# Kernel tuning notes

Hardware: AMD Instinct MI355X
Metric: run time of the kernel (lower is better)

Reference implementation:

```python
import jax, jax.numpy as jnp
import numpy as np

WS = (2, 8, 8)      # window size (wt, wh, ww)
SS = (1, 4, 4)      # shift size
HEADS = 6


def _window_partition(x, ws):
    B, T, H, W, C = x.shape
    wt, wh, ww = ws
    x = x.reshape(B, T // wt, wt, H // wh, wh, W // ww, ww, C)
    x = x.transpose(0, 1, 3, 5, 2, 4, 6, 7)
    return x.reshape(-1, wt * wh * ww, C)  # (B*nW, N, C)


def _window_reverse(w, ws, B, T, H, W):
    wt, wh, ww = ws
    C = w.shape[-1]
    x = w.reshape(B, T // wt, H // wh, W // ww, wt, wh, ww, C)
    x = x.transpose(0, 1, 4, 2, 5, 3, 6, 7)
    return x.reshape(B, T, H, W, C)


def _rel_pos_index(ws):
    wt, wh, ww = ws
    coords = np.stack(np.meshgrid(np.arange(wt), np.arange(wh), np.arange(ww), indexing='ij'))
    coords = coords.reshape(3, -1)                      # (3, N)
    rel = coords[:, :, None] - coords[:, None, :]       # (3, N, N)
    rel = rel.transpose(1, 2, 0).astype(np.int32)
    rel[..., 0] += wt - 1
    rel[..., 1] += wh - 1
    rel[..., 2] += ww - 1
    rel[..., 0] *= (2 * wh - 1) * (2 * ww - 1)
    rel[..., 1] *= (2 * ww - 1)
    return rel.sum(-1)                                  # (N, N)


def _shift_mask(T, H, W, ws, ss):
    # standard Swin shifted-window attention mask
    img = np.zeros((1, T, H, W, 1), dtype=np.float32)
    cnt = 0
    for t in (slice(0, -ws[0]), slice(-ws[0], -ss[0]), slice(-ss[0], None)):
        for h in (slice(0, -ws[1]), slice(-ws[1], -ss[1]), slice(-ss[1], None)):
            for w in (slice(0, -ws[2]), slice(-ws[2], -ss[2]), slice(-ss[2], None)):
                img[:, t, h, w, :] = cnt
                cnt += 1
    mw = np.asarray(_window_partition(jnp.asarray(img), ws)).squeeze(-1)  # (nW, N)
    diff = mw[:, None, :] - mw[:, :, None]
    return jnp.asarray(np.where(diff != 0, -100.0, 0.0).astype(np.float32))


def setup_inputs() -> dict:
    key = jax.random.key(0)
    ks = jax.random.split(key, 9)
    B, T, H, W, C = 2, 8, 64, 64, 192
    hid = 4 * C
    s = 0.02
    x = jax.random.normal(ks[0], (B, T, H, W, C), jnp.float32)
    qkv_w = jax.random.normal(ks[1], (3 * C, C), jnp.float32) * s
    qkv_b = jnp.zeros((3 * C,), jnp.float32)
    proj_w = jax.random.normal(ks[2], (C, C), jnp.float32) * s
    proj_b = jnp.zeros((C,), jnp.float32)
    n_rel = (2 * WS[0] - 1) * (2 * WS[1] - 1) * (2 * WS[2] - 1)
    rpb_table = jax.random.normal(ks[3], (n_rel, HEADS), jnp.float32) * s
    rpb_index = jnp.asarray(_rel_pos_index(WS))
    fc1_w = jax.random.normal(ks[4], (hid, C), jnp.float32) * s
    fc1_b = jnp.zeros((hid,), jnp.float32)
    fc2_w = jax.random.normal(ks[5], (C, hid), jnp.float32) * s
    fc2_b = jnp.zeros((C,), jnp.float32)
    attn_mask = _shift_mask(T, H, W, WS, SS)
    return dict(x=x, attn_mask=attn_mask, qkv_w=qkv_w, qkv_b=qkv_b, proj_w=proj_w,
                proj_b=proj_b, rpb_table=rpb_table, rpb_index=rpb_index,
                fc1_w=fc1_w, fc1_b=fc1_b, fc2_w=fc2_w, fc2_b=fc2_b)


def reference(x, attn_mask, qkv_w, qkv_b, proj_w, proj_b, rpb_table, rpb_index,
              fc1_w, fc1_b, fc2_w, fc2_b):
    B, T, H, W, C = x.shape
    h = HEADS
    d = C // h
    scale = d ** -0.5

    shifted = jnp.roll(x, (-SS[0], -SS[1], -SS[2]), axis=(1, 2, 3))
    xw = _window_partition(shifted, WS)            # (Bn, N, C)
    Bn, N, _ = xw.shape

    qkv = (xw @ qkv_w.T + qkv_b).reshape(Bn, N, 3, h, d).transpose(2, 0, 3, 1, 4)
    q, k, v = qkv[0], qkv[1], qkv[2]               # (Bn, h, N, d)
    attn = jnp.einsum('bhnd,bhmd->bhnm', q * scale, k)
    bias = rpb_table[rpb_index.reshape(-1)].reshape(N, N, h).transpose(2, 0, 1)
    attn = attn + bias[None]
    nW = attn_mask.shape[0]
    attn = (attn.reshape(Bn // nW, nW, h, N, N) + attn_mask[None, :, None]).reshape(Bn, h, N, N)
    attn = jax.nn.softmax(attn, axis=-1)
    out = jnp.einsum('bhnm,bhmd->bhnd', attn, v).transpose(0, 2, 1, 3).reshape(Bn, N, C)
    out = out @ proj_w.T + proj_b

    z = _window_reverse(out, WS, B, T, H, W)
    z = jnp.roll(z, (SS[0], SS[1], SS[2]), axis=(1, 2, 3))

    y = z + x
    mlp = jax.nn.gelu(y @ fc1_w.T + fc1_b, approximate=False) @ fc2_w.T + fc2_b
    return x + mlp
```

## Files before the change

kernel.cpp:

```cpp
#include <hip/hip_runtime.h>
#include <hip/hip_bf16.h>

typedef __attribute__((ext_vector_type(4))) float f32x4;
typedef __attribute__((ext_vector_type(8))) short bf16x8;

#define DEV __device__ __forceinline__

DEV unsigned short f2bf(float f) {
  union { float f; unsigned int u; } v; v.f = f;
  unsigned int r = v.u + 0x7fffu + ((v.u >> 16) & 1u);
  return (unsigned short)(r >> 16);
}

DEV float bf2f(unsigned short u) {
  union { unsigned int u; float f; } v; v.u = ((unsigned int)u) << 16; return v.f;
}

DEV short2 pkbf(float a, float b) {
  float2 t; t.x = a; t.y = b;
  __hip_bfloat162 h = __float22bfloat162_rn(t);
  union { __hip_bfloat162 h; short2 s; } u; u.h = h; return u.s;
}

DEV bf16x8 cvt8(float4 u, float4 v) {
  short2 a = pkbf(u.x, u.y), b = pkbf(u.z, u.w), c = pkbf(v.x, v.y), d = pkbf(v.z, v.w);
  bf16x8 r;
  r[0] = a.x; r[1] = a.y; r[2] = b.x; r[3] = b.y;
  r[4] = c.x; r[5] = c.y; r[6] = d.x; r[7] = d.y;
  return r;
}

DEV float gelu_fast(float v) {
  float u = 1.5957691216057308f * v * (1.0f + 0.044715f * v * v);
  return v / (1.0f + __expf(-u));
}

DEV size_t winmap(int row) {
  int wIdx = row >> 7, n = row & 127;
  int b = wIdx >> 8, widx = wIdx & 255;
  int t = (((widx >> 6) * 2 + (n >> 6)) + 1) & 7;
  int h = ((((widx >> 3) & 7) * 8 + ((n >> 3) & 7)) + 4) & 63;
  int w = (((widx & 7) * 8 + (n & 7)) + 4) & 63;
  return (size_t)(((b * 8 + t) * 64 + h) * 64 + w);
}

DEV int reg3(int tw, int hw, int ww, int n) {
  int ts = tw * 2 + (n >> 6);
  int hs = hw * 8 + ((n >> 3) & 7);
  int wsv = ww * 8 + (n & 7);
  int rt = (ts >= 7) ? 2 : ((ts >= 6) ? 1 : 0);
  int rh = (hs >= 60) ? 2 : ((hs >= 56) ? 1 : 0);
  int rw = (wsv >= 60) ? 2 : ((wsv >= 56) ? 1 : 0);
  return rt * 9 + rh * 3 + rw;
}

DEV void gload16(const unsigned short* g, unsigned short* lds) {
  __builtin_amdgcn_global_load_lds(
      (const __attribute__((address_space(1))) unsigned int*)g,
      (__attribute__((address_space(3))) unsigned int*)lds, 16, 0, 0);
}

__global__ __launch_bounds__(256) void k_prep(
    const float* __restrict__ qkv_w, const float* __restrict__ proj_w,
    const float* __restrict__ fc1_w, const float* __restrict__ fc2_w,
    const float* __restrict__ rpb_t, const int* __restrict__ rpb_i,
    unsigned short* __restrict__ wq, unsigned short* __restrict__ wp,
    unsigned short* __restrict__ w1, unsigned short* __restrict__ w2,
    float* __restrict__ b6) {
  int i = blockIdx.x * 256 + threadIdx.x;
  if (i < 110592) wq[i] = f2bf(qkv_w[i]);
  if (i < 36864)  wp[i] = f2bf(proj_w[i]);
  if (i < 147456) { w1[i] = f2bf(fc1_w[i]); w2[i] = f2bf(fc2_w[i]); }
  if (i < 16384) {
    int idx = rpb_i[i];
    #pragma unroll
    for (int h = 0; h < 6; ++h) b6[h * 16384 + i] = rpb_t[idx * 6 + h];
  }
}

__global__ __launch_bounds__(256) void k_qkv(
    const float* __restrict__ x, const unsigned short* __restrict__ Bm,
    const float* __restrict__ bias, unsigned short* __restrict__ outb) {
  __shared__ char smem[40960];
  float* As = (float*)smem;
  unsigned short* Bs = (unsigned short*)(smem + 32768);
  unsigned short* Cs = (unsigned short*)smem;
  const int tid = threadIdx.x;
  const int wave = tid >> 6, lane = tid & 63;
  const int lin = ((int)blockIdx.x & 7) * 576 + ((int)blockIdx.x >> 3);
  const int mt = lin / 9, nt = lin - mt * 9;
  const int m0 = mt * 128, n0 = nt * 64;
  const int wr = wave >> 1, wc = wave & 1;
  const int l8 = lane >> 3, s8 = lane & 7;

  const float* aptr[8];
  #pragma unroll
  for (int i = 0; i < 8; ++i) {
    int row = wave * 32 + i * 4 + (lane >> 4);
    aptr[i] = x + winmap(m0 + row) * 192 + (((lane & 15) ^ (row & 15)) << 2);
  }

  f32x4 acc[4][2] = {};
  for (int kt = 0; kt < 192; kt += 64) {
    __syncthreads();
    #pragma unroll
    for (int i = 0; i < 8; ++i)
      gload16((const unsigned short*)(aptr[i] + kt), (unsigned short*)(As + (wave * 8 + i) * 256));
    #pragma unroll
    for (int j = 0; j < 2; ++j) {
      int c = wave * 2 + j;
      int row = c * 8 + l8;
      gload16(Bm + (size_t)(n0 + row) * 192 + kt + (s8 ^ l8) * 8, Bs + c * 512);
    }
    __syncthreads();

    #pragma unroll
    for (int kk = 0; kk < 2; ++kk) {
      bf16x8 af[4], bfr[2];
      #pragma unroll
      for (int mi = 0; mi < 4; ++mi) {
        int r = wr * 64 + mi * 16 + (lane & 15);
        int s0 = kk * 8 + (lane >> 4) * 2;
        float4 u = *(const float4*)(As + r * 64 + ((s0 ^ (r & 15)) << 2));
        float4 v = *(const float4*)(As + r * 64 + (((s0 + 1) ^ (r & 15)) << 2));
        af[mi] = cvt8(u, v);
      }
      #pragma unroll
      for (int ni = 0; ni < 2; ++ni) {
        int row = wc * 32 + ni * 16 + (lane & 15);
        int slot = (kk * 4 + (lane >> 4)) ^ (row & 7);
        bfr[ni] = *(const bf16x8*)(Bs + row * 64 + slot * 8);
      }
      #pragma unroll
      for (int mi = 0; mi < 4; ++mi)
        #pragma unroll
        for (int ni = 0; ni < 2; ++ni)
          acc[mi][ni] = __builtin_amdgcn_mfma_f32_16x16x32_bf16(af[mi], bfr[ni], acc[mi][ni], 0, 0, 0);
    }
  }

  __syncthreads();
  #pragma unroll
  for (int ni = 0; ni < 2; ++ni) {
    int coll = wc * 32 + ni * 16 + (lane & 15);
    float bb = bias[n0 + coll];
    #pragma unroll
    for (int mi = 0; mi < 4; ++mi) {
      int rbase = wr * 64 + mi * 16 + ((lane >> 4) << 2);
      #pragma unroll
      for (int j = 0; j < 4; ++j)
        Cs[(rbase + j) * 72 + coll] = f2bf(acc[mi][ni][j] + bb);
    }
  }
  __syncthreads();
  const int row = tid >> 1, hh = tid & 1;
  unsigned short* gb = outb + (size_t)(m0 + row) * 576 + n0 + hh * 32;
  #pragma unroll
  for (int s = 0; s < 4; ++s)
    *(bf16x8*)(gb + s * 8) = *(const bf16x8*)(Cs + row * 72 + hh * 32 + s * 8);
}

enum { EPI_BF16 = 0, EPI_PROJ = 2 };

template <int EPI, int GATHER>
__global__ __launch_bounds__(256) void gemm_bt(
    const void* __restrict__ Ap, const unsigned short* __restrict__ Bm,
    const float* __restrict__ bias, unsigned short* __restrict__ outb,
    const float* __restrict__ xres, int N, int K, int NT) {
  __shared__ unsigned short sh[128 * 72];
  unsigned short* Bs = sh;
  const int tid = threadIdx.x;
  const int wave = tid >> 6, lane = tid & 63;
  const int total = (int)gridDim.x;
  const int lin = ((int)blockIdx.x & 7) * (total >> 3) + ((int)blockIdx.x >> 3);
  const int mt = lin / NT, nt = lin - mt * NT;
  const int m0 = mt * 128, n0 = nt * 64;
  const int wr = wave >> 1, wc = wave & 1;
  const int l8 = lane >> 3, s8 = lane & 7;
  const unsigned short* Ab = (const unsigned short*)Ap;

  size_t abase[4];
  #pragma unroll
  for (int mi = 0; mi < 4; ++mi) {
    int arow = m0 + wr * 64 + mi * 16 + (lane & 15);
    abase[mi] = (size_t)arow * K;
  }

  f32x4 acc[4][2] = {};
  for (int kt = 0; kt < K; kt += 64) {
    __syncthreads();
    #pragma unroll
    for (int i = 0; i < 2; ++i) {
      int c = wave * 2 + i;
      int row = c * 8 + l8;
      gload16(Bm + (size_t)(n0 + row) * K + kt + (s8 ^ l8) * 8, Bs + c * 512);
    }
    __syncthreads();

    #pragma unroll
    for (int kk = 0; kk < 2; ++kk) {
      bf16x8 af[4], bfr[2];
      #pragma unroll
      for (int mi = 0; mi < 4; ++mi)
        af[mi] = *(const bf16x8*)(Ab + abase[mi] + kt + kk * 32 + (lane >> 4) * 8);
      #pragma unroll
      for (int ni = 0; ni < 2; ++ni) {
        int row = wc * 32 + ni * 16 + (lane & 15);
        int slot = (kk * 4 + (lane >> 4)) ^ (row & 7);
        bfr[ni] = *(const bf16x8*)(Bs + row * 64 + slot * 8);
      }
      #pragma unroll
      for (int mi = 0; mi < 4; ++mi)
        #pragma unroll
        for (int ni = 0; ni < 2; ++ni)
          acc[mi][ni] = __builtin_amdgcn_mfma_f32_16x16x32_bf16(af[mi], bfr[ni], acc[mi][ni], 0, 0, 0);
    }
  }

  __syncthreads();
  #pragma unroll
  for (int ni = 0; ni < 2; ++ni) {
    int coll = wc * 32 + ni * 16 + (lane & 15);
    float bb = bias[n0 + coll];
    #pragma unroll
    for (int mi = 0; mi < 4; ++mi) {
      int rbase = wr * 64 + mi * 16 + ((lane >> 4) << 2);
      #pragma unroll
      for (int j = 0; j < 4; ++j)
        sh[(rbase + j) * 72 + coll] = f2bf(acc[mi][ni][j] + bb);
    }
  }
  __syncthreads();
  const int row = tid >> 1, hh = tid & 1;
  if (EPI == EPI_BF16) {
    unsigned short* gb = outb + (size_t)(m0 + row) * N + n0 + hh * 32;
    #pragma unroll
    for (int s = 0; s < 4; ++s)
      *(bf16x8*)(gb + s * 8) = *(const bf16x8*)(sh + row * 72 + hh * 32 + s * 8);
  } else {
    size_t gf = winmap(m0 + row) * 192 + n0 + hh * 32;
    #pragma unroll
    for (int s = 0; s < 4; ++s) {
      bf16x8 cv = *(const bf16x8*)(sh + row * 72 + hh * 32 + s * 8);
      float4 x0 = *(const float4*)(xres + gf + s * 8);
      float4 x1 = *(const float4*)(xres + gf + s * 8 + 4);
      bf16x8 o;
      o[0] = (short)f2bf(bf2f((unsigned short)cv[0]) + x0.x);
      o[1] = (short)f2bf(bf2f((unsigned short)cv[1]) + x0.y);
      o[2] = (short)f2bf(bf2f((unsigned short)cv[2]) + x0.z);
      o[3] = (short)f2bf(bf2f((unsigned short)cv[3]) + x0.w);
      o[4] = (short)f2bf(bf2f((unsigned short)cv[4]) + x1.x);
      o[5] = (short)f2bf(bf2f((unsigned short)cv[5]) + x1.y);
      o[6] = (short)f2bf(bf2f((unsigned short)cv[6]) + x1.z);
      o[7] = (short)f2bf(bf2f((unsigned short)cv[7]) + x1.w);
      *(bf16x8*)(outb + gf + s * 8) = o;
    }
  }
}

__global__ __launch_bounds__(256) void k_attn(const unsigned short* __restrict__ qkv,
                                              const float* __restrict__ bias6,
                                              unsigned short* __restrict__ attn_out) {
  __shared__ unsigned short Kl[128 * 40];
  __shared__ unsigned short Vt[32 * 136];
  __shared__ unsigned short Pl[128 * 140];
  const int lin = ((int)blockIdx.x & 7) * 384 + ((int)blockIdx.x >> 3);
  const int wIdx = lin / 6;
  const int hd = lin - wIdx * 6;
  const int tid = threadIdx.x;
  const int wave = tid >> 6, lane = tid & 63;
  const int widx = wIdx & 255;
  const int tw = widx >> 6, hw = (widx >> 3) & 7, ww = widx & 7;
  const size_t qbase = (size_t)wIdx * 73728;

  #pragma unroll
  for (int r = 0; r < 2; ++r) {
    int idx = r * 256 + tid;
    int row = idx >> 2, slot = idx & 3;
    *(bf16x8*)(Kl + row * 40 + slot * 8) =
        *(const bf16x8*)(qkv + qbase + (size_t)row * 576 + 192 + hd * 32 + slot * 8);
  }
  if (tid < 128) {
    #pragma unroll
    for (int slot = 0; slot < 4; ++slot) {
      bf16x8 v = *(const bf16x8*)(qkv + qbase + (size_t)tid * 576 + 384 + hd * 32 + slot * 8);
      #pragma unroll
      for (int j = 0; j < 8; ++j)
        Vt[(slot * 8 + j) * 136 + tid] = (unsigned short)v[j];
    }
  }
  bf16x8 qf[2];
  #pragma unroll
  for (int tr = 0; tr < 2; ++tr)
    qf[tr] = *(const bf16x8*)(qkv + qbase +
                              (size_t)(wave * 32 + tr * 16 + (lane & 15)) * 576 +
                              hd * 32 + (lane >> 4) * 8);
  int rcol[8];
  #pragma unroll
  for (int tc = 0; tc < 8; ++tc) rcol[tc] = reg3(tw, hw, ww, tc * 16 + (lane & 15));
  __syncthreads();

  f32x4 s[2][8];
  #pragma unroll
  for (int tc = 0; tc < 8; ++tc) {
    bf16x8 kf = *(const bf16x8*)(Kl + (tc * 16 + (lane & 15)) * 40 + (lane >> 4) * 8);
    #pragma unroll
    for (int tr = 0; tr < 2; ++tr) {
      f32x4 z = {0.f, 0.f, 0.f, 0.f};
      s[tr][tc] = __builtin_amdgcn_mfma_f32_16x16x32_bf16(qf[tr], kf, z, 0, 0, 0);
    }
  }

  const float scale = 0.17677669529663687f;
  float rsum[2][4];
  #pragma unroll
  for (int tr = 0; tr < 2; ++tr) {
    #pragma unroll
    for (int j = 0; j < 4; ++j) {
      int row = wave * 32 + tr * 16 + ((lane >> 4) << 2) + j;
      const float* bp = bias6 + hd * 16384 + row * 128;
      int rrow = reg3(tw, hw, ww, row);
      float mx = -1e30f;
      #pragma unroll
      for (int tc = 0; tc < 8; ++tc) {
        int col = tc * 16 + (lane & 15);
        float v = s[tr][tc][j] * scale + bp[col] + ((rrow == rcol[tc]) ? 0.0f : -100.0f);
        s[tr][tc][j] = v;
        mx = fmaxf(mx, v);
      }
      #pragma unroll
      for (int d = 1; d < 16; d <<= 1) mx = fmaxf(mx, __shfl_xor(mx, d));
      float sum = 0.f;
      #pragma unroll
      for (int tc = 0; tc < 8; ++tc) {
        float p = __expf(s[tr][tc][j] - mx);
        s[tr][tc][j] = p;
        sum += p;
      }
      #pragma unroll
      for (int d = 1; d < 16; d <<= 1) sum += __shfl_xor(sum, d);
      rsum[tr][j] = sum;
      #pragma unroll
      for (int tc = 0; tc < 8; ++tc)
        Pl[row * 140 + tc * 16 + (lane & 15)] = f2bf(s[tr][tc][j]);
    }
  }
  __syncthreads();

  f32x4 o[2][2] = {};
  #pragma unroll
  for (int ks = 0; ks < 4; ++ks) {
    bf16x8 pa[2], vb[2];
    #pragma unroll
    for (int tr = 0; tr < 2; ++tr)
      pa[tr] = *(const bf16x8*)(Pl + (wave * 32 + tr * 16 + (lane & 15)) * 140 +
                                ks * 32 + (lane >> 4) * 8);
    #pragma unroll
    for (int nc = 0; nc < 2; ++nc)
      vb[nc] = *(const bf16x8*)(Vt + (nc * 16 + (lane & 15)) * 136 +
                                ks * 32 + (lane >> 4) * 8);
    #pragma unroll
    for (int tr = 0; tr < 2; ++tr)
      #pragma unroll
      for (int nc = 0; nc < 2; ++nc)
        o[tr][nc] = __builtin_amdgcn_mfma_f32_16x16x32_bf16(pa[tr], vb[nc], o[tr][nc], 0, 0, 0);
  }

  #pragma unroll
  for (int tr = 0; tr < 2; ++tr)
    #pragma unroll
    for (int nc = 0; nc < 2; ++nc)
      #pragma unroll
      for (int j = 0; j < 4; ++j) {
        int row = wave * 32 + tr * 16 + ((lane >> 4) << 2) + j;
        float v = o[tr][nc][j] * (1.0f / rsum[tr][j]);
        attn_out[((size_t)wIdx * 128 + row) * 192 + hd * 32 + nc * 16 + (lane & 15)] = f2bf(v);
      }
}

__global__ __launch_bounds__(512) void k_mlp(
    const unsigned short* __restrict__ y, const unsigned short* __restrict__ w1,
    const float* __restrict__ b1, const unsigned short* __restrict__ w2,
    const float* __restrict__ b2, const float* __restrict__ xin,
    float* __restrict__ out) {
  __shared__ unsigned short Ys[3 * 8192];
  __shared__ unsigned short W1s[3 * 4096];
  __shared__ unsigned short W2s[192 * 64];
  __shared__ unsigned short Hs[128 * 64];
  const int tid = threadIdx.x;
  const int wave = tid >> 6, lane = tid & 63;
  const int l8 = lane >> 3, s8 = lane & 7;
  const int m0 = (int)blockIdx.x * 128;
  const int w1r = wave >> 1, w1c = wave & 1;
  const int w2r = wave >> 2, w2c = wave & 3;

  #pragma unroll
  for (int i = 0; i < 6; ++i) {
    int c = wave * 6 + i;
    int p = c >> 4, q = c & 15;
    int row = q * 8 + l8;
    gload16(y + (size_t)(m0 + row) * 192 + p * 64 + (s8 ^ l8) * 8, Ys + p * 8192 + q * 512);
  }
  #pragma unroll
  for (int i = 0; i < 3; ++i) {
    int c = wave * 3 + i;
    int p = c >> 3, q = c & 7;
    gload16(w1 + (size_t)(q * 8 + l8) * 192 + p * 64 + (s8 ^ l8) * 8, W1s + p * 4096 + q * 512);
    gload16(w2 + (size_t)(c * 8 + l8) * 768 + (s8 ^ l8) * 8, W2s + c * 512);
  }
  __syncthreads();

  f32x4 oacc[4][3] = {};
  for (int ch = 0; ch < 12; ++ch) {
    const int hb = ch * 64;
    f32x4 hacc[2][2] = {};
    #pragma unroll
    for (int kk = 0; kk < 6; ++kk) {
      int p = kk >> 1, half = kk & 1;
      bf16x8 af[2], bfr[2];
      #pragma unroll
      for (int mi = 0; mi < 2; ++mi) {
        int r = w1r * 32 + mi * 16 + (lane & 15);
        int slot = (half * 4 + (lane >> 4)) ^ (r & 7);
        af[mi] = *(const bf16x8*)(Ys + p * 8192 + r * 64 + slot * 8);
      }
      #pragma unroll
      for (int ni = 0; ni < 2; ++ni) {
        int n = w1c * 32 + ni * 16 + (lane & 15);
        int slot = (half * 4 + (lane >> 4)) ^ (n & 7);
        bfr[ni] = *(const bf16x8*)(W1s + p * 4096 + n * 64 + slot * 8);
      }
      #pragma unroll
      for (int mi = 0; mi < 2; ++mi)
        #pragma unroll
        for (int ni = 0; ni < 2; ++ni)
          hacc[mi][ni] = __builtin_amdgcn_mfma_f32_16x16x32_bf16(af[mi], bfr[ni], hacc[mi][ni], 0, 0, 0);
    }
    __syncthreads();

    #pragma unroll
    for (int ni = 0; ni < 2; ++ni) {
      int coll = w1c * 32 + ni * 16 + (lane & 15);
      float bb = b1[hb + coll];
      #pragma unroll
      for (int mi = 0; mi < 2; ++mi) {
        int rbase = w1r * 32 + mi * 16 + ((lane >> 4) << 2);
        #pragma unroll
        for (int j = 0; j < 4; ++j) {
          int r = rbase + j;
          Hs[r * 64 + (((coll >> 3) ^ (r & 7)) * 8) + (coll & 7)] = f2bf(gelu_fast(hacc[mi][ni][j] + bb));
        }
      }
    }
    if (ch < 11) {
      #pragma unroll
      for (int i = 0; i < 3; ++i) {
        int c = wave * 3 + i;
        int p = c >> 3, q = c & 7;
        gload16(w1 + (size_t)(hb + 64 + q * 8 + l8) * 192 + p * 64 + (s8 ^ l8) * 8,
                W1s + p * 4096 + q * 512);
      }
    }
    __syncthreads();

    #pragma unroll
    for (int kk = 0; kk < 2; ++kk) {
      bf16x8 pa[4], vb[3];
      #pragma unroll
      for (int mi = 0; mi < 4; ++mi) {
        int r = w2r * 64 + mi * 16 + (lane & 15);
        int slot = (kk * 4 + (lane >> 4)) ^ (r & 7);
        pa[mi] = *(const bf16x8*)(Hs + r * 64 + slot * 8);
      }
      #pragma unroll
      for (int ni = 0; ni < 3; ++ni) {
        int n = w2c * 48 + ni * 16 + (lane & 15);
        int slot = (kk * 4 + (lane >> 4)) ^ (n & 7);
        vb[ni] = *(const bf16x8*)(W2s + n * 64 + slot * 8);
      }
      #pragma unroll
      for (int mi = 0; mi < 4; ++mi)
        #pragma unroll
        for (int ni = 0; ni < 3; ++ni)
          oacc[mi][ni] = __builtin_amdgcn_mfma_f32_16x16x32_bf16(pa[mi], vb[ni], oacc[mi][ni], 0, 0, 0);
    }
    __syncthreads();
    if (ch < 11) {
      #pragma unroll
      for (int i = 0; i < 3; ++i) {
        int c = wave * 3 + i;
        gload16(w2 + (size_t)(c * 8 + l8) * 768 + hb + 64 + (s8 ^ l8) * 8, W2s + c * 512);
      }
    }
  }

  #pragma unroll
  for (int ni = 0; ni < 3; ++ni) {
    int col = w2c * 48 + ni * 16 + (lane & 15);
    float bb = b2[col];
    #pragma unroll
    for (int mi = 0; mi < 4; ++mi) {
      int rbase = m0 + w2r * 64 + mi * 16 + ((lane >> 4) << 2);
      #pragma unroll
      for (int j = 0; j < 4; ++j) {
        size_t idx = (size_t)(rbase + j) * 192 + col;
        out[idx] = xin[idx] + oacc[mi][ni][j] + bb;
      }
    }
  }
}

extern "C" void kernel_launch(void* const* d_in, const int* in_sizes, int n_in,
                              void* d_out, int out_size, void* d_ws, size_t ws_size,
                              hipStream_t stream) {
  const float* x      = (const float*)d_in[0];
  const float* qkv_w  = (const float*)d_in[2];
  const float* qkv_b  = (const float*)d_in[3];
  const float* proj_w = (const float*)d_in[4];
  const float* proj_b = (const float*)d_in[5];
  const float* rpb_t  = (const float*)d_in[6];
  const int*   rpb_i  = (const int*)d_in[7];
  const float* fc1_w  = (const float*)d_in[8];
  const float* fc1_b  = (const float*)d_in[9];
  const float* fc2_w  = (const float*)d_in[10];
  const float* fc2_b  = (const float*)d_in[11];
  float* out = (float*)d_out;
  char* ws = (char*)d_ws;

  unsigned short* qkv = (unsigned short*)(ws + 0);
  unsigned short* att = (unsigned short*)(ws + 75497472);
  unsigned short* ybf = (unsigned short*)(ws + 100663296);
  unsigned short* wq  = (unsigned short*)(ws + 125829120);
  unsigned short* wp  = (unsigned short*)(ws + 126050304);
  unsigned short* w1  = (unsigned short*)(ws + 126124032);
  unsigned short* w2  = (unsigned short*)(ws + 126418944);
  float*          b6  = (float*)(ws + 126713856);

  k_prep<<<576, 256, 0, stream>>>(qkv_w, proj_w, fc1_w, fc2_w, rpb_t, rpb_i, wq, wp, w1, w2, b6);
  k_qkv<<<4608, 256, 0, stream>>>(x, wq, qkv_b, qkv);
  k_attn<<<3072, 256, 0, stream>>>(qkv, b6, att);
  gemm_bt<EPI_PROJ, 0><<<1536, 256, 0, stream>>>(att, wp, proj_b, ybf, x, 192, 192, 3);
  k_mlp<<<512, 512, 0, stream>>>(ybf, w1, fc1_b, w2, fc2_b, x, out);
}
```

Before: 217.0 us.

## Read MLP weights directly from global, transpose fc1 GEMM, and raise occupancy

The MLP kernel no longer stages fc1/fc2 weight tiles in shared memory. MFMA weight fragments are now read straight from global memory, where the small weight matrices should stay cached in L2. The first GEMM is computed transposed (hidden x token), so each lane holds four consecutive hidden units. These are GELU'd, packed to bf16 and written to the H tile with one 8-byte swizzled store instead of scalar stores. Removing the weight tiles shrinks shared memory and drops one barrier and the per-chunk weight refill, and launch bounds now ask for higher occupancy. The costs are more global/L2 traffic per MFMA and more latency exposed on the weight loads. Separately, the attention kernel spreads the V-transpose load over all 256 threads instead of 128.

```diff
diff --git a/kernel.cpp b/kernel.cpp
--- a/kernel.cpp
+++ b/kernel.cpp
@@ -280,13 +280,15 @@
     *(bf16x8*)(Kl + row * 40 + slot * 8) =
         *(const bf16x8*)(qkv + qbase + (size_t)row * 576 + 192 + hd * 32 + slot * 8);
   }
-  if (tid < 128) {
-    #pragma unroll
-    for (int slot = 0; slot < 4; ++slot) {
-      bf16x8 v = *(const bf16x8*)(qkv + qbase + (size_t)tid * 576 + 384 + hd * 32 + slot * 8);
+  {
+    int vtok = tid & 127, shalf = tid >> 7;
+    #pragma unroll
+    for (int so = 0; so < 2; ++so) {
+      int slot = shalf * 2 + so;
+      bf16x8 v = *(const bf16x8*)(qkv + qbase + (size_t)vtok * 576 + 384 + hd * 32 + slot * 8);
       #pragma unroll
       for (int j = 0; j < 8; ++j)
-        Vt[(slot * 8 + j) * 136 + tid] = (unsigned short)v[j];
+        Vt[(slot * 8 + j) * 136 + vtok] = (unsigned short)v[j];
     }
   }
   bf16x8 qf[2];
@@ -378,20 +380,19 @@
       }
 }
 
-__global__ __launch_bounds__(512) void k_mlp(
+__global__ __launch_bounds__(512, 4) void k_mlp(
     const unsigned short* __restrict__ y, const unsigned short* __restrict__ w1,
     const float* __restrict__ b1, const unsigned short* __restrict__ w2,
     const float* __restrict__ b2, const float* __restrict__ xin,
     float* __restrict__ out) {
   __shared__ unsigned short Ys[3 * 8192];
-  __shared__ unsigned short W1s[3 * 4096];
-  __shared__ unsigned short W2s[192 * 64];
   __shared__ unsigned short Hs[128 * 64];
   const int tid = threadIdx.x;
   const int wave = tid >> 6, lane = tid & 63;
   const int l8 = lane >> 3, s8 = lane & 7;
+  const int lrow = lane & 15, lk = lane >> 4;
   const int m0 = (int)blockIdx.x * 128;
-  const int w1r = wave >> 1, w1c = wave & 1;
+  const int wh = wave >> 2, wt = wave & 3;
   const int w2r = wave >> 2, w2c = wave & 3;
 
   #pragma unroll
@@ -401,13 +402,6 @@
     int row = q * 8 + l8;
     gload16(y + (size_t)(m0 + row) * 192 + p * 64 + (s8 ^ l8) * 8, Ys + p * 8192 + q * 512);
   }
-  #pragma unroll
-  for (int i = 0; i < 3; ++i) {
-    int c = wave * 3 + i;
-    int p = c >> 3, q = c & 7;
-    gload16(w1 + (size_t)(q * 8 + l8) * 192 + p * 64 + (s8 ^ l8) * 8, W1s + p * 4096 + q * 512);
-    gload16(w2 + (size_t)(c * 8 + l8) * 768 + (s8 ^ l8) * 8, W2s + c * 512);
-  }
   __syncthreads();
 
   f32x4 oacc[4][3] = {};
@@ -419,46 +413,37 @@
       int p = kk >> 1, half = kk & 1;
       bf16x8 af[2], bfr[2];
       #pragma unroll
-      for (int mi = 0; mi < 2; ++mi) {
-        int r = w1r * 32 + mi * 16 + (lane & 15);
-        int slot = (half * 4 + (lane >> 4)) ^ (r & 7);
-        af[mi] = *(const bf16x8*)(Ys + p * 8192 + r * 64 + slot * 8);
-      }
-      #pragma unroll
-      for (int ni = 0; ni < 2; ++ni) {
-        int n = w1c * 32 + ni * 16 + (lane & 15);
-        int slot = (half * 4 + (lane >> 4)) ^ (n & 7);
-        bfr[ni] = *(const bf16x8*)(W1s + p * 4096 + n * 64 + slot * 8);
-      }
-      #pragma unroll
-      for (int mi = 0; mi < 2; ++mi)
+      for (int hi = 0; hi < 2; ++hi) {
+        int hrow = hb + wh * 32 + hi * 16 + lrow;
+        af[hi] = *(const bf16x8*)(w1 + (size_t)hrow * 192 + kk * 32 + lk * 8);
+      }
+      #pragma unroll
+      for (int ti = 0; ti < 2; ++ti) {
+        int r = wt * 32 + ti * 16 + lrow;
+        int slot = (half * 4 + lk) ^ (r & 7);
+        bfr[ti] = *(const bf16x8*)(Ys + p * 8192 + r * 64 + slot * 8);
+      }
+      #pragma unroll
+      for (int hi = 0; hi < 2; ++hi)
         #pragma unroll
-        for (int ni = 0; ni < 2; ++ni)
-          hacc[mi][ni] = __builtin_amdgcn_mfma_f32_16x16x32_bf16(af[mi], bfr[ni], hacc[mi][ni], 0, 0, 0);
+        for (int ti = 0; ti < 2; ++ti)
+          hacc[hi][ti] = __builtin_amdgcn_mfma_f32_16x16x32_bf16(af[hi], bfr[ti], hacc[hi][ti], 0, 0, 0);
     }
     __syncthreads();
 
     #pragma unroll
-    for (int ni = 0; ni < 2; ++ni) {
-      int coll = w1c * 32 + ni * 16 + (lane & 15);
-      float bb = b1[hb + coll];
-      #pragma unroll
-      for (int mi = 0; mi < 2; ++mi) {
-        int rbase = w1r * 32 + mi * 16 + ((lane >> 4) << 2);
-        #pragma unroll
-        for (int j = 0; j < 4; ++j) {
-          int r = rbase + j;
-          Hs[r * 64 + (((coll >> 3) ^ (r & 7)) * 8) + (coll & 7)] = f2bf(gelu_fast(hacc[mi][ni][j] + bb));
-        }
-      }
-    }
-    if (ch < 11) {
-      #pragma unroll
-      for (int i = 0; i < 3; ++i) {
-        int c = wave * 3 + i;
-        int p = c >> 3, q = c & 7;
-        gload16(w1 + (size_t)(hb + 64 + q * 8 + l8) * 192 + p * 64 + (s8 ^ l8) * 8,
-                W1s + p * 4096 + q * 512);
+    for (int hi = 0; hi < 2; ++hi) {
+      int hid4 = wh * 8 + hi * 4 + lk;
+      float4 bb = *(const float4*)(b1 + hb + hid4 * 4);
+      #pragma unroll
+      for (int ti = 0; ti < 2; ++ti) {
+        int tok = wt * 32 + ti * 16 + lrow;
+        short2 p01 = pkbf(gelu_fast(hacc[hi][ti][0] + bb.x), gelu_fast(hacc[hi][ti][1] + bb.y));
+        short2 p23 = pkbf(gelu_fast(hacc[hi][ti][2] + bb.z), gelu_fast(hacc[hi][ti][3] + bb.w));
+        ushort4 o;
+        o.x = (unsigned short)p01.x; o.y = (unsigned short)p01.y;
+        o.z = (unsigned short)p23.x; o.w = (unsigned short)p23.y;
+        *(ushort4*)(Hs + tok * 64 + ((hid4 ^ (tok & 14)) << 2)) = o;
       }
     }
     __syncthreads();
@@ -468,15 +453,14 @@
       bf16x8 pa[4], vb[3];
       #pragma unroll
       for (int mi = 0; mi < 4; ++mi) {
-        int r = w2r * 64 + mi * 16 + (lane & 15);
-        int slot = (kk * 4 + (lane >> 4)) ^ (r & 7);
-        pa[mi] = *(const bf16x8*)(Hs + r * 64 + slot * 8);
+        int tok = w2r * 64 + mi * 16 + lrow;
+        int s = kk * 8 + lk * 2;
+        pa[mi] = *(const bf16x8*)(Hs + tok * 64 + ((s ^ (tok & 14)) << 2));
       }
       #pragma unroll
       for (int ni = 0; ni < 3; ++ni) {
-        int n = w2c * 48 + ni * 16 + (lane & 15);
-        int slot = (kk * 4 + (lane >> 4)) ^ (n & 7);
-        vb[ni] = *(const bf16x8*)(W2s + n * 64 + slot * 8);
+        int n = w2c * 48 + ni * 16 + lrow;
+        vb[ni] = *(const bf16x8*)(w2 + (size_t)n * 768 + hb + kk * 32 + lk * 8);
       }
       #pragma unroll
       for (int mi = 0; mi < 4; ++mi)
@@ -484,23 +468,15 @@
         for (int ni = 0; ni < 3; ++ni)
           oacc[mi][ni] = __builtin_amdgcn_mfma_f32_16x16x32_bf16(pa[mi], vb[ni], oacc[mi][ni], 0, 0, 0);
     }
-    __syncthreads();
-    if (ch < 11) {
-      #pragma unroll
-      for (int i = 0; i < 3; ++i) {
-        int c = wave * 3 + i;
-        gload16(w2 + (size_t)(c * 8 + l8) * 768 + hb + 64 + (s8 ^ l8) * 8, W2s + c * 512);
-      }
-    }
   }
 
   #pragma unroll
   for (int ni = 0; ni < 3; ++ni) {
-    int col = w2c * 48 + ni * 16 + (lane & 15);
+    int col = w2c * 48 + ni * 16 + lrow;
     float bb = b2[col];
     #pragma unroll
     for (int mi = 0; mi < 4; ++mi) {
-      int rbase = m0 + w2r * 64 + mi * 16 + ((lane >> 4) << 2);
+      int rbase = m0 + w2r * 64 + mi * 16 + (lk << 2);
       #pragma unroll
       for (int j = 0; j < 4; ++j) {
         size_t idx = (size_t)(rbase + j) * 192 + col;
```

Result: slower. 246.2 us (+13.4%).
